# Performance work log

Measured on AMD Instinct MI355X. Metric: run time of the kernel, lower is better.

The kernel has to match this reference:

```python
import jax, jax.numpy as jnp
import numpy as np

SCALING = 32.0 / 16  # alpha / rank


def setup_inputs() -> dict:
    key = jax.random.key(0)
    k1, k2, k3, k4, k5 = jax.random.split(key, 5)
    B, S, IN, OUT, R = 4, 2048, 4096, 4096, 16
    x = jax.random.normal(k1, (B, S, IN), dtype=jnp.float32)
    weight = jax.random.normal(k2, (OUT, IN), dtype=jnp.float32) * 0.02
    lora_a_w = jax.random.normal(k3, (R, IN), dtype=jnp.float32) * 0.02
    lora_b_w = jax.random.normal(k4, (OUT, R), dtype=jnp.float32) * 0.02
    magnitude = jax.random.uniform(k5, (OUT,), dtype=jnp.float32) + 0.5
    return {"x": x, "weight": weight, "lora_a_w": lora_a_w,
            "lora_b_w": lora_b_w, "magnitude": magnitude}


def reference(x, weight, lora_a_w, lora_b_w, magnitude):
    # base linear: x @ W^T  -> [..., out_dim]
    base_out = jnp.einsum('bsi,oi->bso', x, weight)
    # low-rank path (dropout is identity at p=0.0)
    lora_out = jnp.einsum('bsr,or->bso', jnp.einsum('bsi,ri->bsr', x, lora_a_w), lora_b_w)
    # merged low-rank weight B @ A (torch uses an eye-matrix trick; direct matmul is equivalent)
    lora_weight = lora_b_w @ lora_a_w  # [out, in]
    # row-wise norm of adapted weight; detached in the original
    weight_norm = jax.lax.stop_gradient(
        jnp.linalg.norm(weight + SCALING * lora_weight, axis=1))  # [out]
    mag_norm_scale = (magnitude / weight_norm)[None, None, :]  # [1,1,out]
    dora_out = (mag_norm_scale - 1.0) * base_out + mag_norm_scale * lora_out * SCALING
    return dora_out + base_out
```

## Files before the change

kernel.cpp:

```cpp
#include <hip/hip_runtime.h>
#include <hip/hip_bf16.h>
#include <stdint.h>

#define M_DIM 8192
#define N_DIM 4096
#define K_DIM 4096
#define R_DIM 16
#define NT    64

#define WPREP_BLOCKS 4096
#define CAST_BLOCKS  4096

typedef __attribute__((ext_vector_type(8))) short bf16x8;
typedef __attribute__((ext_vector_type(4))) float f32x4;

__device__ __forceinline__ unsigned short f2bf(float f) {
  union { float f; unsigned int u; } v; v.f = f;
  unsigned int r = 0x7FFFu + ((v.u >> 16) & 1u);
  return (unsigned short)((v.u + r) >> 16);
}

__device__ __forceinline__ void gload16(const unsigned short* g, unsigned short* l) {
  __builtin_amdgcn_global_load_lds(
      (const __attribute__((address_space(1))) void*)g,
      (__attribute__((address_space(3))) void*)l,
      16, 0, 0);
}

__global__ void __launch_bounds__(256) prep_kernel(
    const float4* __restrict__ x4, ushort4* __restrict__ xbf4,
    const float4* __restrict__ W4, const float4* __restrict__ Aw4,
    const float* __restrict__ Bw, const float* __restrict__ mag,
    ushort4* __restrict__ wbf4, float* __restrict__ scale) {
  const int tid = threadIdx.x;

  if (blockIdx.x >= WPREP_BLOCKS) {
    const int base = (blockIdx.x - WPREP_BLOCKS) * 2048 + tid;
    #pragma unroll
    for (int u = 0; u < 8; ++u) {
      const int i = base + u * 256;
      float4 f = x4[i];
      ushort4 o;
      o.x = f2bf(f.x); o.y = f2bf(f.y); o.z = f2bf(f.z); o.w = f2bf(f.w);
      xbf4[i] = o;
    }
    return;
  }

  const int o = blockIdx.x;
  float Bo[R_DIM];
  #pragma unroll
  for (int r = 0; r < R_DIM; ++r) Bo[r] = Bw[o * R_DIM + r] * 2.0f;

  float ss = 0.f;
  #pragma unroll
  for (int g = 0; g < 4; ++g) {
    const int c = g * 256 + tid;
    float4 v = W4[(size_t)o * 1024 + c];
    #pragma unroll
    for (int r = 0; r < R_DIM; ++r) {
      const float4 a = Aw4[(size_t)r * 1024 + c];
      const float b = Bo[r];
      v.x += b * a.x; v.y += b * a.y; v.z += b * a.z; v.w += b * a.w;
    }
    ss += v.x * v.x + v.y * v.y + v.z * v.z + v.w * v.w;
    ushort4 ov;
    ov.x = f2bf(v.x); ov.y = f2bf(v.y); ov.z = f2bf(v.z); ov.w = f2bf(v.w);
    wbf4[(size_t)o * 1024 + c] = ov;
  }

  __shared__ float red[4];
  #pragma unroll
  for (int off = 32; off > 0; off >>= 1) ss += __shfl_down(ss, off, 64);
  if ((tid & 63) == 0) red[tid >> 6] = ss;
  __syncthreads();
  if (tid == 0)
    scale[o] = mag[o] / sqrtf(red[0] + red[1] + red[2] + red[3]);
}

__global__ void __launch_bounds__(512, 2)
dora_gemm(const unsigned short* __restrict__ A,
          const unsigned short* __restrict__ Bt,
          const float* __restrict__ scale,
          float* __restrict__ C) {
  __shared__ __align__(16) unsigned short As[2][2][128 * 64];
  __shared__ __align__(16) unsigned short Bs[2][2][128 * 64];

  const int tid  = threadIdx.x;
  const int lane = tid & 63;
  const int wave = tid >> 6;

  const int fid = blockIdx.y * gridDim.x + blockIdx.x;
  const int s   = (fid & 7) * 64 + (fid >> 3);
  const int bM  = (s >> 4) * 256;
  const int bN  = (s & 15) * 256;

  const int l3  = lane >> 3;
  const int l7  = lane & 7;
  const int swz = (l7 ^ l3) * 8;
  const int w8  = wave * 8;

  const unsigned short* srcA = A  + (size_t)(bM + w8 + l3) * K_DIM + swz;
  const unsigned short* srcB = Bt + (size_t)(bN + (wave & 3) * 8 + l3 + 64 * (wave >> 2)) * K_DIM + swz;

  const int fr   = lane & 15;
  const int fq   = lane >> 4;
  const int fr7  = fr & 7;
  const int arow = fr + 64 * (wave >> 2);
  const int brow = fr + 32 * (wave & 3);

  f32x4 acc[8][4];
  #pragma unroll
  for (int i = 0; i < 8; ++i)
    #pragma unroll
    for (int j = 0; j < 4; ++j) acc[i][j] = (f32x4){0.f, 0.f, 0.f, 0.f};

  bf16x8 aF[4][2];
  bf16x8 bF0[2][2];
  bf16x8 bF1[2][2];

#define STAGE_A(cc, hh, k0) do {                                              \
    gload16(srcA + (size_t)((hh) * 64)       * K_DIM + (k0), (unsigned short*)&As[cc][hh][w8 * 64]);        \
    gload16(srcA + (size_t)((hh) * 64 + 128) * K_DIM + (k0), (unsigned short*)&As[cc][hh][(64 + w8) * 64]); \
  } while (0)
#define STAGE_B(cc, hh, k0) do {                                              \
    gload16(srcB + (size_t)((hh) * 32)       * K_DIM + (k0), (unsigned short*)&Bs[cc][hh][w8 * 64]);        \
    gload16(srcB + (size_t)((hh) * 32 + 128) * K_DIM + (k0), (unsigned short*)&Bs[cc][hh][(64 + w8) * 64]); \
  } while (0)
#define LOAD_A(cc, mh) do {                                                   \
    _Pragma("unroll")                                                         \
    for (int mt = 0; mt < 4; ++mt) {                                          \
      _Pragma("unroll")                                                       \
      for (int h = 0; h < 2; ++h)                                             \
        aF[mt][h] = *(const bf16x8*)&As[cc][mh][(arow + mt * 16) * 64 + (((h * 4 + fq) ^ fr7) * 8)]; \
    }                                                                         \
  } while (0)
#define LOAD_B(cc, nh, dst) do {                                              \
    _Pragma("unroll")                                                         \
    for (int nt = 0; nt < 2; ++nt) {                                          \
      _Pragma("unroll")                                                       \
      for (int h = 0; h < 2; ++h)                                             \
        dst[nt][h] = *(const bf16x8*)&Bs[cc][nh][(brow + nt * 16) * 64 + (((h * 4 + fq) ^ fr7) * 8)]; \
    }                                                                         \
  } while (0)
#define MFMA_Q(mh, nh, bfr) do {                                              \
    _Pragma("unroll")                                                         \
    for (int mt = 0; mt < 4; ++mt) {                                          \
      _Pragma("unroll")                                                       \
      for (int nt = 0; nt < 2; ++nt) {                                        \
        _Pragma("unroll")                                                     \
        for (int h = 0; h < 2; ++h)                                           \
          acc[(mh) * 4 + mt][(nh) * 2 + nt] = __builtin_amdgcn_mfma_f32_16x16x32_bf16( \
              aF[mt][h], bfr[nt][h], acc[(mh) * 4 + mt][(nh) * 2 + nt], 0, 0, 0); \
      }                                                                       \
    }                                                                         \
  } while (0)
#define PH_SYNC_IN()  do { __builtin_amdgcn_s_barrier();                       \
    asm volatile("s_waitcnt lgkmcnt(0)" ::: "memory"); } while (0)

#define GROUP(cc, tt) do {                                                    \
                                                      \
    LOAD_A(cc, 0); LOAD_B(cc, 0, bF0);                                        \
    if ((tt) + 1 < NT) STAGE_A((cc) ^ 1, 1, ((tt) + 1) * 64);                 \
    PH_SYNC_IN();                                                             \
    __builtin_amdgcn_s_setprio(1); MFMA_Q(0, 0, bF0); __builtin_amdgcn_s_setprio(0); \
    __builtin_amdgcn_s_barrier();                                             \
                                                      \
    LOAD_B(cc, 1, bF1);                                                       \
    if ((tt) + 1 < NT) STAGE_B((cc) ^ 1, 1, ((tt) + 1) * 64);                 \
    PH_SYNC_IN();                                                             \
    __builtin_amdgcn_s_setprio(1); MFMA_Q(0, 1, bF1); __builtin_amdgcn_s_setprio(0); \
    __builtin_amdgcn_s_barrier();                                             \
                                                      \
    LOAD_A(cc, 1);                                                            \
    if ((tt) + 2 < NT) STAGE_A(cc, 0, ((tt) + 2) * 64);                       \
    PH_SYNC_IN();                                                             \
    __builtin_amdgcn_s_setprio(1); MFMA_Q(1, 0, bF0); __builtin_amdgcn_s_setprio(0); \
    __builtin_amdgcn_s_barrier();                                             \
                                                      \
    if ((tt) + 2 < NT) STAGE_B(cc, 0, ((tt) + 2) * 64);                       \
    PH_SYNC_IN();                                                             \
    __builtin_amdgcn_s_setprio(1); MFMA_Q(1, 1, bF1); __builtin_amdgcn_s_setprio(0); \
    if ((tt) < NT - 2) asm volatile("s_waitcnt vmcnt(4)" ::: "memory");       \
    else               asm volatile("s_waitcnt vmcnt(0)" ::: "memory");       \
    __builtin_amdgcn_s_barrier();                                             \
  } while (0)

  STAGE_A(0, 0, 0); STAGE_B(0, 0, 0);
  STAGE_A(0, 1, 0); STAGE_B(0, 1, 0);
  STAGE_A(1, 0, 64); STAGE_B(1, 0, 64);
  asm volatile("s_waitcnt vmcnt(4)" ::: "memory");
  __builtin_amdgcn_s_barrier();

  for (int t = 0; t < NT; t += 2) {
    GROUP(0, t);
    GROUP(1, t + 1);
  }

#undef GROUP
#undef PH_SYNC_IN
#undef MFMA_Q
#undef LOAD_B
#undef LOAD_A
#undef STAGE_B
#undef STAGE_A

  const int wMo = (wave >> 2) * 128;
  const int wNo = (wave & 3) * 64;
  float scv[4];
  #pragma unroll
  for (int fn = 0; fn < 4; ++fn) scv[fn] = scale[bN + wNo + fn * 16 + fr];
  #pragma unroll
  for (int fm = 0; fm < 8; ++fm) {
    const int m0 = bM + wMo + fm * 16 + fq * 4;
    #pragma unroll
    for (int fn = 0; fn < 4; ++fn) {
      const int n = bN + wNo + fn * 16 + fr;
      #pragma unroll
      for (int r = 0; r < 4; ++r)
        C[(size_t)(m0 + r) * N_DIM + n] = acc[fm][fn][r] * scv[fn];
    }
  }
}

extern "C" void kernel_launch(void* const* d_in, const int* in_sizes, int n_in,
                              void* d_out, int out_size, void* d_ws, size_t ws_size,
                              hipStream_t stream) {
  const float* x   = (const float*)d_in[0];
  const float* W   = (const float*)d_in[1];
  const float* la  = (const float*)d_in[2];
  const float* lb  = (const float*)d_in[3];
  const float* mag = (const float*)d_in[4];
  float* out = (float*)d_out;

  unsigned short* xbf = (unsigned short*)d_ws;
  unsigned short* wbf = (unsigned short*)((char*)d_ws + (size_t)M_DIM * K_DIM * 2);
  float* scale = (float*)((char*)d_ws + (size_t)M_DIM * K_DIM * 2 + (size_t)N_DIM * K_DIM * 2);

  prep_kernel<<<WPREP_BLOCKS + CAST_BLOCKS, 256, 0, stream>>>(
      (const float4*)x, (ushort4*)xbf, (const float4*)W, (const float4*)la,
      lb, mag, (ushort4*)wbf, scale);
  dim3 grid(N_DIM / 256, M_DIM / 256);
  dora_gemm<<<grid, 512, 0, stream>>>(xbf, wbf, scale, out);
}
```

Baseline: 551.9 us.

## Batch weight-prep rows per block and deepen GEMM prefetch pipeline

The weight-prep path now handles 32 output rows per block. Each thread loads its 16 LoRA-A columns once into registers and reuses them across those rows, instead of re-reading A for every row, and the per-row norm reductions are batched at the end. The GEMM main loop is restaged so all four sub-tiles of k-step t+2 are issued within a group, using explicit vmcnt waits and a peeled tail, which keeps more global loads in flight. The cost is higher register pressure in prep (32 accumulators plus 64 floats of A) and a more fragile wait-count schedule.

```diff
diff --git a/kernel.cpp b/kernel.cpp
--- a/kernel.cpp
+++ b/kernel.cpp
@@ -8,8 +8,9 @@
 #define R_DIM 16
 #define NT    64
 
-#define WPREP_BLOCKS 4096
-#define CAST_BLOCKS  4096
+#define WROWS    32
+#define WBLOCKS  (N_DIM / WROWS)
+#define CAST_BLOCKS 4096
 
 typedef __attribute__((ext_vector_type(8))) short bf16x8;
 typedef __attribute__((ext_vector_type(4))) float f32x4;
@@ -33,9 +34,11 @@
     const float* __restrict__ Bw, const float* __restrict__ mag,
     ushort4* __restrict__ wbf4, float* __restrict__ scale) {
   const int tid = threadIdx.x;
-
-  if (blockIdx.x >= WPREP_BLOCKS) {
-    const int base = (blockIdx.x - WPREP_BLOCKS) * 2048 + tid;
+  __shared__ float BoL[WROWS * R_DIM];
+  __shared__ float red[4][WROWS];
+
+  if (blockIdx.x >= WBLOCKS) {
+    const int base = (blockIdx.x - WBLOCKS) * 2048 + tid;
     #pragma unroll
     for (int u = 0; u < 8; ++u) {
       const int i = base + u * 256;
@@ -47,36 +50,59 @@
     return;
   }
 
-  const int o = blockIdx.x;
-  float Bo[R_DIM];
-  #pragma unroll
-  for (int r = 0; r < R_DIM; ++r) Bo[r] = Bw[o * R_DIM + r] * 2.0f;
-
-  float ss = 0.f;
-  #pragma unroll
-  for (int g = 0; g < 4; ++g) {
-    const int c = g * 256 + tid;
-    float4 v = W4[(size_t)o * 1024 + c];
-    #pragma unroll
-    for (int r = 0; r < R_DIM; ++r) {
-      const float4 a = Aw4[(size_t)r * 1024 + c];
-      const float b = Bo[r];
-      v.x += b * a.x; v.y += b * a.y; v.z += b * a.z; v.w += b * a.w;
+  const int o0 = blockIdx.x * WROWS;
+  for (int i = tid; i < WROWS * R_DIM; i += 256)
+    BoL[i] = Bw[o0 * R_DIM + i] * 2.0f;
+  __syncthreads();
+
+  float ssa[WROWS];
+  #pragma unroll
+  for (int r = 0; r < WROWS; ++r) ssa[r] = 0.f;
+
+  for (int ch = 0; ch < 4; ++ch) {
+    const int c = ch * 256 + tid;
+    float4 a[R_DIM];
+    #pragma unroll
+    for (int r = 0; r < R_DIM; ++r) a[r] = Aw4[(size_t)r * 1024 + c];
+
+    #pragma unroll
+    for (int row = 0; row < WROWS; ++row) {
+      float4 v = W4[(size_t)(o0 + row) * 1024 + c];
+      const float4 b0 = *(const float4*)&BoL[row * R_DIM + 0];
+      const float4 b1 = *(const float4*)&BoL[row * R_DIM + 4];
+      const float4 b2 = *(const float4*)&BoL[row * R_DIM + 8];
+      const float4 b3 = *(const float4*)&BoL[row * R_DIM + 12];
+#define FMA4(bb, ar) { v.x += (bb)*(ar).x; v.y += (bb)*(ar).y; v.z += (bb)*(ar).z; v.w += (bb)*(ar).w; }
+      FMA4(b0.x, a[0])  FMA4(b0.y, a[1])  FMA4(b0.z, a[2])  FMA4(b0.w, a[3])
+      FMA4(b1.x, a[4])  FMA4(b1.y, a[5])  FMA4(b1.z, a[6])  FMA4(b1.w, a[7])
+      FMA4(b2.x, a[8])  FMA4(b2.y, a[9])  FMA4(b2.z, a[10]) FMA4(b2.w, a[11])
+      FMA4(b3.x, a[12]) FMA4(b3.y, a[13]) FMA4(b3.z, a[14]) FMA4(b3.w, a[15])
+#undef FMA4
+      ssa[row] += v.x * v.x + v.y * v.y + v.z * v.z + v.w * v.w;
+      ushort4 ov;
+      ov.x = f2bf(v.x); ov.y = f2bf(v.y); ov.z = f2bf(v.z); ov.w = f2bf(v.w);
+      wbf4[(size_t)(o0 + row) * 1024 + c] = ov;
     }
-    ss += v.x * v.x + v.y * v.y + v.z * v.z + v.w * v.w;
-    ushort4 ov;
-    ov.x = f2bf(v.x); ov.y = f2bf(v.y); ov.z = f2bf(v.z); ov.w = f2bf(v.w);
-    wbf4[(size_t)o * 1024 + c] = ov;
-  }
-
-  __shared__ float red[4];
-  #pragma unroll
-  for (int off = 32; off > 0; off >>= 1) ss += __shfl_down(ss, off, 64);
-  if ((tid & 63) == 0) red[tid >> 6] = ss;
+  }
+
+  const int lane = tid & 63;
+  const int wave = tid >> 6;
+  #pragma unroll
+  for (int row = 0; row < WROWS; ++row) {
+    float v = ssa[row];
+    #pragma unroll
+    for (int off = 32; off > 0; off >>= 1) v += __shfl_down(v, off, 64);
+    if (lane == 0) red[wave][row] = v;
+  }
   __syncthreads();
-  if (tid == 0)
-    scale[o] = mag[o] / sqrtf(red[0] + red[1] + red[2] + red[3]);
-}
+  if (tid < WROWS) {
+    const float s = red[0][tid] + red[1][tid] + red[2][tid] + red[3][tid];
+    scale[o0 + tid] = mag[o0 + tid] / sqrtf(s);
+  }
+}
+
+#define VMCNT_(n) asm volatile("s_waitcnt vmcnt(" #n ")" ::: "memory")
+#define VMCNT(n) VMCNT_(n)
 
 __global__ void __launch_bounds__(512, 2)
 dora_gemm(const unsigned short* __restrict__ A,
@@ -155,49 +181,55 @@
       }                                                                       \
     }                                                                         \
   } while (0)
-#define PH_SYNC_IN()  do { __builtin_amdgcn_s_barrier();                       \
+#define PH_SYNC_IN()  do { __builtin_amdgcn_s_barrier();                      \
     asm volatile("s_waitcnt lgkmcnt(0)" ::: "memory"); } while (0)
-
-#define GROUP(cc, tt) do {                                                    \
-                                                      \
+#define PRIO1 __builtin_amdgcn_s_setprio(1)
+#define PRIO0 __builtin_amdgcn_s_setprio(0)
+
+#define GROUP(cc, tt, STG, W1N, W4N) do {                                     \
+                                                                      \
     LOAD_A(cc, 0); LOAD_B(cc, 0, bF0);                                        \
-    if ((tt) + 1 < NT) STAGE_A((cc) ^ 1, 1, ((tt) + 1) * 64);                 \
-    PH_SYNC_IN();                                                             \
-    __builtin_amdgcn_s_setprio(1); MFMA_Q(0, 0, bF0); __builtin_amdgcn_s_setprio(0); \
-    __builtin_amdgcn_s_barrier();                                             \
-                                                      \
+    PH_SYNC_IN();                                                             \
+    PRIO1; MFMA_Q(0, 0, bF0); PRIO0;                                          \
+    VMCNT(W1N);                                                               \
+    __builtin_amdgcn_s_barrier();                                             \
+                                                                      \
     LOAD_B(cc, 1, bF1);                                                       \
-    if ((tt) + 1 < NT) STAGE_B((cc) ^ 1, 1, ((tt) + 1) * 64);                 \
-    PH_SYNC_IN();                                                             \
-    __builtin_amdgcn_s_setprio(1); MFMA_Q(0, 1, bF1); __builtin_amdgcn_s_setprio(0); \
-    __builtin_amdgcn_s_barrier();                                             \
-                                                      \
+    if (STG) STAGE_A(cc, 0, ((tt) + 2) * 64);                                 \
+    PH_SYNC_IN();                                                             \
+    PRIO1; MFMA_Q(0, 1, bF1); PRIO0;                                          \
+    __builtin_amdgcn_s_barrier();                                             \
+                                                                      \
     LOAD_A(cc, 1);                                                            \
-    if ((tt) + 2 < NT) STAGE_A(cc, 0, ((tt) + 2) * 64);                       \
-    PH_SYNC_IN();                                                             \
-    __builtin_amdgcn_s_setprio(1); MFMA_Q(1, 0, bF0); __builtin_amdgcn_s_setprio(0); \
-    __builtin_amdgcn_s_barrier();                                             \
-                                                      \
-    if ((tt) + 2 < NT) STAGE_B(cc, 0, ((tt) + 2) * 64);                       \
-    PH_SYNC_IN();                                                             \
-    __builtin_amdgcn_s_setprio(1); MFMA_Q(1, 1, bF1); __builtin_amdgcn_s_setprio(0); \
-    if ((tt) < NT - 2) asm volatile("s_waitcnt vmcnt(4)" ::: "memory");       \
-    else               asm volatile("s_waitcnt vmcnt(0)" ::: "memory");       \
-    __builtin_amdgcn_s_barrier();                                             \
-  } while (0)
-
-  STAGE_A(0, 0, 0); STAGE_B(0, 0, 0);
-  STAGE_A(0, 1, 0); STAGE_B(0, 1, 0);
+    if (STG) STAGE_B(cc, 0, ((tt) + 2) * 64);                                 \
+    PH_SYNC_IN();                                                             \
+    PRIO1; MFMA_Q(1, 0, bF0); PRIO0;                                          \
+    __builtin_amdgcn_s_barrier();                                             \
+                                                                      \
+    if (STG) { STAGE_A(cc, 1, ((tt) + 2) * 64); STAGE_B(cc, 1, ((tt) + 2) * 64); } \
+    PH_SYNC_IN();                                                             \
+    PRIO1; MFMA_Q(1, 1, bF1); PRIO0;                                          \
+    VMCNT(W4N);                                                               \
+    __builtin_amdgcn_s_barrier();                                             \
+  } while (0)
+
+  STAGE_A(0, 0, 0);  STAGE_B(0, 0, 0);
+  STAGE_A(0, 1, 0);  STAGE_B(0, 1, 0);
   STAGE_A(1, 0, 64); STAGE_B(1, 0, 64);
-  asm volatile("s_waitcnt vmcnt(4)" ::: "memory");
+  STAGE_A(1, 1, 64); STAGE_B(1, 1, 64);
+  VMCNT(12);
   __builtin_amdgcn_s_barrier();
 
-  for (int t = 0; t < NT; t += 2) {
-    GROUP(0, t);
-    GROUP(1, t + 1);
-  }
+  for (int t = 0; t < NT - 2; t += 2) {
+    GROUP(0, t, 1, 8, 12);
+    GROUP(1, t + 1, 1, 8, 12);
+  }
+  GROUP(0, NT - 2, 0, 8, 4);
+  GROUP(1, NT - 1, 0, 0, 0);
 
 #undef GROUP
+#undef PRIO0
+#undef PRIO1
 #undef PH_SYNC_IN
 #undef MFMA_Q
 #undef LOAD_B
@@ -237,7 +269,7 @@
   unsigned short* wbf = (unsigned short*)((char*)d_ws + (size_t)M_DIM * K_DIM * 2);
   float* scale = (float*)((char*)d_ws + (size_t)M_DIM * K_DIM * 2 + (size_t)N_DIM * K_DIM * 2);
 
-  prep_kernel<<<WPREP_BLOCKS + CAST_BLOCKS, 256, 0, stream>>>(
+  prep_kernel<<<WBLOCKS + CAST_BLOCKS, 256, 0, stream>>>(
       (const float4*)x, (ushort4*)xbf, (const float4*)W, (const float4*)la,
       lb, mag, (ushort4*)wbf, scale);
   dim3 grid(N_DIM / 256, M_DIM / 256);
```

Result: slower. 661.3 us (+19.8%).
